# Performance work log

Hardware: AMD Instinct MI355X
Metric: run time of the kernel (lower is better)

## Reference

```python
import jax, jax.numpy as jnp
import numpy as np

B, C, H, W = 8, 256, 128, 128
J = 8          # number of segmentation classes / fc_mu layers
S = 256        # style_length
EPS = 1e-5


def _conv3x3(x, w, b):
    # x: [B,S,H,W], w: [C,S,3,3] (OIHW), padding=1 -> SAME
    y = jax.lax.conv_general_dilated(
        x, w, window_strides=(1, 1), padding='SAME',
        dimension_numbers=('NCHW', 'OIHW', 'NCHW'))
    return y + b[None, :, None, None]


def setup_inputs() -> dict:
    key = jax.random.key(0)
    ks = jax.random.split(key, 12)
    fp = jax.random.normal(ks[0], (B, C, H, W), dtype=jnp.float32)
    # one-hot segmentation map (nearest-interpolated seg maps are one-hot)
    labels = jax.random.randint(ks[1], (B, H, W), 0, J)
    sg = jnp.transpose(jax.nn.one_hot(labels, J, dtype=jnp.float32), (0, 3, 1, 2))
    style_codes = jax.random.normal(ks[2], (B, J + 1, S), dtype=jnp.float32)
    mask_codes = jax.random.randint(ks[3], (B, J), 0, 2).astype(jnp.int32)
    # parameters
    bn_weight = jnp.ones((C,), jnp.float32)
    bn_bias = jnp.zeros((C,), jnp.float32)
    conv_gamma_w = jax.random.normal(ks[4], (C, S, 3, 3), jnp.float32) * 0.02
    conv_gamma_b = jnp.zeros((C,), jnp.float32)
    conv_beta_w = jax.random.normal(ks[5], (C, S, 3, 3), jnp.float32) * 0.02
    conv_beta_b = jnp.zeros((C,), jnp.float32)
    fc_w = jax.random.normal(ks[6], (J, S, S), jnp.float32) * 0.02  # [j, out, in]
    fc_b = jnp.zeros((J, S), jnp.float32)
    return dict(fp=fp, sg=sg, style_codes=style_codes, mask_codes=mask_codes,
                bn_weight=bn_weight, bn_bias=bn_bias,
                conv_gamma_w=conv_gamma_w, conv_gamma_b=conv_gamma_b,
                conv_beta_w=conv_beta_w, conv_beta_b=conv_beta_b,
                fc_w=fc_w, fc_b=fc_b)


def reference(fp, sg, style_codes, mask_codes, bn_weight, bn_bias,
              conv_gamma_w, conv_gamma_b, conv_beta_w, conv_beta_b,
              fc_w, fc_b):
    # BatchNorm2d (training-mode batch statistics, affine)
    mean = jnp.mean(fp, axis=(0, 2, 3), keepdims=True)
    var = jnp.var(fp, axis=(0, 2, 3), keepdims=True)
    xn = (fp - mean) * jax.lax.rsqrt(var + EPS)
    xn = xn * bn_weight[None, :, None, None] + bn_bias[None, :, None, None]

    nJ = sg.shape[1]
    # style code selection: j if mask_codes[b,j]==1 else nJ (the extra/shared code)
    idx = jnp.where(mask_codes == 1, jnp.arange(nJ)[None, :], nJ)        # [B,J]
    codes = jnp.take_along_axis(style_codes, idx[:, :, None], axis=1)    # [B,J,S]
    # per-region Linear (weights differ per region j) + ReLU
    mu = jax.nn.relu(jnp.einsum('bjs,jts->bjt', codes, fc_w) + fc_b[None])  # [B,J,S]
    # masked scatter of per-region style vectors (sg is one-hot -> exact)
    middle = jnp.einsum('bjhw,bjs->bshw', sg, mu)                         # [B,S,H,W]

    gamma = _conv3x3(middle, conv_gamma_w, conv_gamma_b)
    beta = _conv3x3(middle, conv_beta_w, conv_beta_b)
    return xn * (1.0 + gamma) + beta
```

## Files before the change

kernel.cpp:

```cpp
#include <hip/hip_runtime.h>
#include <hip/hip_fp16.h>
#include <stdint.h>

#define NB 8
#define NC 256
#define NH 128
#define NW 128
#define NJ 8
#define NS 256
#define NHW (NH*NW)
#define BN_EPS 1e-5f
#define TSTRIDE 68

__device__ inline __half2 u2h(uint32_t u) {
    union { uint32_t u; __half2 h; } x; x.u = u; return x.h;
}
__device__ inline uint32_t h2u(__half2 h) {
    union { uint32_t u; __half2 h; } x; x.h = h; return x.u;
}

__global__ __launch_bounds__(256) void kA(
        const float* __restrict__ fp, float* __restrict__ psum, float* __restrict__ psq,
        const float* __restrict__ sg, uint8_t* __restrict__ lab,
        const float* __restrict__ style, const int* __restrict__ mask,
        const float* __restrict__ fcw, const float* __restrict__ fcb,
        float* __restrict__ mu,
        const float* __restrict__ wg, const float* __restrict__ wb,
        uint32_t* __restrict__ wpk) {
    __shared__ float ls[4], lq[4];
    __shared__ float code[NS];
    __shared__ uint32_t tileu[32][65];
    int blk = blockIdx.x;
    int t = threadIdx.x;
    if (blk < 512) {
        int pix = blk * 256 + t;
        int b = pix >> 14, hw = pix & 16383;
        const float* base = sg + (size_t)b * NJ * NHW + hw;
        int l = 0;
        #pragma unroll
        for (int j = 0; j < NJ; j++)
            if (base[(size_t)j * NHW] > 0.5f) l = j;
        lab[pix] = (uint8_t)l;
    } else if (blk < 576) {
        int bj = blk - 512;
        int b = bj >> 3, j = bj & 7;
        int row = (mask[bj] == 1) ? j : NJ;
        code[t] = style[((size_t)b * (NJ + 1) + row) * NS + t];
        __syncthreads();
        const float4* w4 = (const float4*)(fcw + ((size_t)j * NS + t) * NS);
        const float4* c4 = (const float4*)code;
        float acc = fcb[j * NS + t];
        for (int s4 = 0; s4 < NS / 4; s4++) {
            float4 wv = w4[s4];
            float4 cv = c4[s4];
            acc += wv.x * cv.x + wv.y * cv.y + wv.z * cv.z + wv.w * cv.w;
        }
        mu[bj * NS + t] = fmaxf(acc, 0.f);
    } else if (blk < 864) {
        int i = blk - 576;
        int skc = i % 72, cc = i / 72;
        int sk0 = skc * 32, c0 = cc * 64;
        {
            int skl = t & 31, cl = t >> 5;
            #pragma unroll
            for (int p = 0; p < 8; p++) {
                int c = c0 + cl + p * 8;
                float g  = __builtin_nontemporal_load(&wg[(size_t)c * 2304 + sk0 + skl]);
                float b2 = __builtin_nontemporal_load(&wb[(size_t)c * 2304 + sk0 + skl]);
                tileu[skl][cl + p * 8] = h2u(__floats2half2_rn(g, b2));
            }
        }
        __syncthreads();
        {
            int cl = t & 63, skl = t >> 6;
            #pragma unroll
            for (int p = 0; p < 8; p++) {
                int sk = sk0 + skl + p * 4;
                int s = sk / 9, k = sk - s * 9;
                wpk[(size_t)k * (NS * NC) + (size_t)s * NC + c0 + cl] = tileu[skl + p * 4][cl];
            }
        }
    } else {
        int bc = blk - 864;
        int b = bc >> 8, c = bc & 255;
        const float4* p = (const float4*)(fp + (size_t)(b * NC + c) * NHW);
        float s = 0.f, q = 0.f;
        for (int i = t; i < NHW / 4; i += 256) {
            float4 v = p[i];
            s += v.x + v.y + v.z + v.w;
            q += v.x * v.x + v.y * v.y + v.z * v.z + v.w * v.w;
        }
        for (int o = 32; o > 0; o >>= 1) {
            s += __shfl_down(s, o);
            q += __shfl_down(q, o);
        }
        int wid = t >> 6, lane = t & 63;
        if (lane == 0) { ls[wid] = s; lq[wid] = q; }
        __syncthreads();
        if (t == 0) {
            float S2 = 0.f, Q2 = 0.f;
            for (int i = 0; i < 4; i++) { S2 += ls[i]; Q2 += lq[i]; }
            psum[c * 8 + b] = S2;
            psq[c * 8 + b] = Q2;
        }
    }
}

__global__ __launch_bounds__(1024) void kB(
        const float* __restrict__ psum, const float* __restrict__ psq,
        const float* __restrict__ bnw, const float* __restrict__ bnb,
        const float* __restrict__ cgb, const float* __restrict__ cbb,
        float2* __restrict__ Al, uint32_t* __restrict__ Bl,
        const float* __restrict__ mu, const uint32_t* __restrict__ wpk,
        uint32_t* __restrict__ T) {
    int blk = blockIdx.x;
    int t = threadIdx.x;
    if (blk == 72) {
        if (t < 256) {
            int c = t;
            float s = 0.f, q = 0.f;
            for (int b = 0; b < NB; b++) { s += psum[c * 8 + b]; q += psq[c * 8 + b]; }
            const float N = (float)(NB * NHW);
            float mean = s / N;
            float var = q / N - mean * mean;
            if (var < 0.f) var = 0.f;
            float inv = 1.0f / sqrtf(var + BN_EPS);
            float a = bnw[c] * inv;
            float b2 = bnb[c] - mean * a;
            Al[c] = make_float2(a, b2);
            Bl[c] = h2u(__floats2half2_rn(1.0f + cgb[c], cbb[c]));
        }
        return;
    }
    int b = blk / 9, k = blk - b * 9;
    __shared__ float ms[NS * NJ];
    for (int i = t; i < NJ * NS; i += 1024) {
        int j = i >> 8, s = i & 255;
        ms[s * 8 + j] = mu[(size_t)b * NJ * NS + i];
    }
    __syncthreads();
    int c = t & 255, jq = t >> 8;
    int j0 = jq * 2;
    const uint32_t* wp = wpk + (size_t)k * NS * NC + c;
    float g0 = 0.f, be0 = 0.f, g1 = 0.f, be1 = 0.f;
    for (int s = 0; s < NS; s++) {
        float2 w2 = __half22float2(u2h(wp[(size_t)s * NC]));
        float2 mm = *(const float2*)&ms[s * 8 + j0];
        g0  += mm.x * w2.x;  be0 += mm.x * w2.y;
        g1  += mm.y * w2.x;  be1 += mm.y * w2.y;
    }
    uint32_t* o = T + ((size_t)b * 9 + k) * 9 * NC + c;
    o[(size_t)j0 * NC]       = h2u(__floats2half2_rn(g0, be0));
    o[(size_t)(j0 + 1) * NC] = h2u(__floats2half2_rn(g1, be1));
    if (jq == 0) o[(size_t)8 * NC] = 0u;
}

#define TAP_TREE(FLD, OUT)                                              \
    {                                                                   \
        __half2 p01 = __hadd2(u2h(tv[0].FLD), u2h(tv[1].FLD));          \
        __half2 p23 = __hadd2(u2h(tv[2].FLD), u2h(tv[3].FLD));          \
        __half2 p45 = __hadd2(u2h(tv[4].FLD), u2h(tv[5].FLD));          \
        __half2 p67 = __hadd2(u2h(tv[6].FLD), u2h(tv[7].FLD));          \
        __half2 p8b = __hadd2(u2h(tv[8].FLD), u2h(bias.FLD));           \
        OUT = __hadd2(__hadd2(__hadd2(p01, p23), __hadd2(p45, p67)), p8b); \
    }

__global__ __launch_bounds__(256, 5) void k_main(
        const float* __restrict__ fp, const uint8_t* __restrict__ lab,
        const uint32_t* __restrict__ T, const float2* __restrict__ Ag,
        const uint32_t* __restrict__ Bg, float* __restrict__ out) {
    int blk = blockIdx.x;
    int cc = blk & 3;
    int h  = (blk >> 2) & 127;
    int b  = blk >> 9;
    int c0 = cc * 64;

    __shared__ uint32_t Tl[81 * TSTRIDE];
    __shared__ float2   Apl[64];
    __shared__ uint32_t Bpl[64];
    __shared__ uint8_t  Ll[3][NW];

    int t = threadIdx.x;
    {
        const uint32_t* Tg = T + (size_t)b * 81 * NC + c0;
        int rr = t >> 4, ii = (t & 15) * 4;
        #pragma unroll
        for (int pass = 0; pass < 5; pass++) {
            int r = rr + pass * 16;
            *(uint4*)&Tl[r * TSTRIDE + ii] = *(const uint4*)&Tg[(size_t)r * NC + ii];
        }
        if (t < 16) *(uint4*)&Tl[80 * TSTRIDE + t * 4] = *(const uint4*)&Tg[(size_t)80 * NC + t * 4];
    }
    if (t < 64) { Apl[t] = Ag[c0 + t]; Bpl[t] = Bg[c0 + t]; }
    if (t >= 128 && t < 224) {
        int tt = t - 128;
        int r = tt >> 5, q = tt & 31;
        int hr = h - 1 + r;
        uint32_t v = 0;
        if (hr >= 0 && hr < NH)
            v = ((const uint32_t*)(lab + (size_t)b * NHW + (size_t)hr * NW))[q];
        ((uint32_t*)Ll)[tt] = v;
    }
    __syncthreads();

    int w = t & 127, cg = t >> 7;
    int base_k[9];
    #pragma unroll
    for (int dy = 0; dy < 3; dy++) {
        int hr = h - 1 + dy;
        bool rok = (hr >= 0) && (hr < NH);
        #pragma unroll
        for (int dx = 0; dx < 3; dx++) {
            int ww = w - 1 + dx;
            bool ok = rok && (ww >= 0) && (ww < NW);
            int wc = ww < 0 ? 0 : (ww > NW - 1 ? NW - 1 : ww);
            int j = ok ? (int)Ll[dy][wc] : 8;
            int k = dy * 3 + dx;
            base_k[k] = (k * 9 + j) * TSTRIDE + cg * 32;
        }
    }

    const float* fpb = fp + ((size_t)b * NC + c0 + cg * 32) * NHW + (size_t)h * NW + w;
    float*       ob  = out + ((size_t)b * NC + c0 + cg * 32) * NHW + (size_t)h * NW + w;

    #pragma unroll
    for (int q = 0; q < 8; q++) {
        float x0 = fpb[(size_t)(q * 4 + 0) * NHW];
        float x1 = fpb[(size_t)(q * 4 + 1) * NHW];
        float x2 = fpb[(size_t)(q * 4 + 2) * NHW];
        float x3 = fpb[(size_t)(q * 4 + 3) * NHW];
        uint4 tv[9];
        #pragma unroll
        for (int k = 0; k < 9; k++)
            tv[k] = *(const uint4*)&Tl[base_k[k] + q * 4];
        uint4 bias = *(const uint4*)&Bpl[cg * 32 + q * 4];
        __half2 a0, a1, a2, a3;
        TAP_TREE(x, a0);
        TAP_TREE(y, a1);
        TAP_TREE(z, a2);
        TAP_TREE(w, a3);
        float4 ap01 = *(const float4*)&Apl[cg * 32 + q * 4];
        float4 ap23 = *(const float4*)&Apl[cg * 32 + q * 4 + 2];
        float2 g0 = __half22float2(a0);
        float2 g1 = __half22float2(a1);
        float2 g2 = __half22float2(a2);
        float2 g3 = __half22float2(a3);
        __builtin_nontemporal_store((x0 * ap01.x + ap01.y) * g0.x + g0.y, &ob[(size_t)(q * 4 + 0) * NHW]);
        __builtin_nontemporal_store((x1 * ap01.z + ap01.w) * g1.x + g1.y, &ob[(size_t)(q * 4 + 1) * NHW]);
        __builtin_nontemporal_store((x2 * ap23.x + ap23.y) * g2.x + g2.y, &ob[(size_t)(q * 4 + 2) * NHW]);
        __builtin_nontemporal_store((x3 * ap23.z + ap23.w) * g3.x + g3.y, &ob[(size_t)(q * 4 + 3) * NHW]);
    }
}

extern "C" void kernel_launch(void* const* d_in, const int* in_sizes, int n_in,
                              void* d_out, int out_size, void* d_ws, size_t ws_size,
                              hipStream_t stream) {
    const float* fp    = (const float*)d_in[0];
    const float* sg    = (const float*)d_in[1];
    const float* style = (const float*)d_in[2];
    const int*   mask  = (const int*)d_in[3];
    const float* bnw   = (const float*)d_in[4];
    const float* bnb   = (const float*)d_in[5];
    const float* cgw   = (const float*)d_in[6];
    const float* cgb   = (const float*)d_in[7];
    const float* cbw   = (const float*)d_in[8];
    const float* cbb   = (const float*)d_in[9];
    const float* fcw   = (const float*)d_in[10];
    const float* fcb   = (const float*)d_in[11];
    float* out = (float*)d_out;

    char* ws = (char*)d_ws;
    float*    psum = (float*)(ws + 0);
    float*    psq  = (float*)(ws + 8192);
    float2*   Al   = (float2*)(ws + 16384);
    uint32_t* Bl   = (uint32_t*)(ws + 18432);
    uint8_t*  lab  = (uint8_t*)(ws + 19456);
    float*    mu   = (float*)(ws + 150528);
    uint32_t* wpk  = (uint32_t*)(ws + 216064);
    uint32_t* T    = (uint32_t*)(ws + 2575360);

    hipLaunchKernelGGL(kA, dim3(2912), dim3(256), 0, stream,
                       fp, psum, psq, sg, lab, style, mask, fcw, fcb, mu,
                       cgw, cbw, wpk);
    hipLaunchKernelGGL(kB, dim3(73), dim3(1024), 0, stream,
                       psum, psq, bnw, bnb, cgb, cbb, Al, Bl, mu, wpk, T);
    hipLaunchKernelGGL(k_main, dim3(NB * NH * 4), dim3(256), 0, stream,
                       fp, lab, T, Al, Bl, out);
}
```

Before: 85.13 us.

## Split conv-tap table between LDS and global loads, add nontemporal hints

Moves the last three of the nine conv-tap table rows out of shared memory, loading them per thread straight from global/L2 with a one-step software prefetch across the q loop. This shrinks the LDS staging footprint and the LDS read traffic per output, aiming for more occupancy and less LDS-bound time. The cost is extra global gathers and more registers. Separately, the label and FC-weight reads in the prologue kernel now use nontemporal loads.

```diff
diff --git a/kernel.cpp b/kernel.cpp
--- a/kernel.cpp
+++ b/kernel.cpp
@@ -11,6 +11,8 @@
 #define NHW (NH*NW)
 #define BN_EPS 1e-5f
 #define TSTRIDE 68
+
+typedef float f4v __attribute__((ext_vector_type(4)));
 
 __device__ inline __half2 u2h(uint32_t u) {
     union { uint32_t u; __half2 h; } x; x.u = u; return x.h;
@@ -39,7 +41,7 @@
         int l = 0;
         #pragma unroll
         for (int j = 0; j < NJ; j++)
-            if (base[(size_t)j * NHW] > 0.5f) l = j;
+            if (__builtin_nontemporal_load(&base[(size_t)j * NHW]) > 0.5f) l = j;
         lab[pix] = (uint8_t)l;
     } else if (blk < 576) {
         int bj = blk - 512;
@@ -47,12 +49,12 @@
         int row = (mask[bj] == 1) ? j : NJ;
         code[t] = style[((size_t)b * (NJ + 1) + row) * NS + t];
         __syncthreads();
-        const float4* w4 = (const float4*)(fcw + ((size_t)j * NS + t) * NS);
-        const float4* c4 = (const float4*)code;
+        const f4v* w4 = (const f4v*)(fcw + ((size_t)j * NS + t) * NS);
+        const f4v* c4 = (const f4v*)code;
         float acc = fcb[j * NS + t];
         for (int s4 = 0; s4 < NS / 4; s4++) {
-            float4 wv = w4[s4];
-            float4 cv = c4[s4];
+            f4v wv = __builtin_nontemporal_load(&w4[s4]);
+            f4v cv = c4[s4];
             acc += wv.x * cv.x + wv.y * cv.y + wv.z * cv.z + wv.w * cv.w;
         }
         mu[bj * NS + t] = fmaxf(acc, 0.f);
@@ -160,8 +162,8 @@
         __half2 p01 = __hadd2(u2h(tv[0].FLD), u2h(tv[1].FLD));          \
         __half2 p23 = __hadd2(u2h(tv[2].FLD), u2h(tv[3].FLD));          \
         __half2 p45 = __hadd2(u2h(tv[4].FLD), u2h(tv[5].FLD));          \
-        __half2 p67 = __hadd2(u2h(tv[6].FLD), u2h(tv[7].FLD));          \
-        __half2 p8b = __hadd2(u2h(tv[8].FLD), u2h(bias.FLD));           \
+        __half2 p67 = __hadd2(u2h(gt0.FLD), u2h(gt1.FLD));              \
+        __half2 p8b = __hadd2(u2h(gt2.FLD), u2h(bias.FLD));             \
         OUT = __hadd2(__hadd2(__hadd2(p01, p23), __hadd2(p45, p67)), p8b); \
     }
 
@@ -175,21 +177,18 @@
     int b  = blk >> 9;
     int c0 = cc * 64;
 
-    __shared__ uint32_t Tl[81 * TSTRIDE];
+    __shared__ uint32_t Tl[54 * TSTRIDE];
     __shared__ float2   Apl[64];
     __shared__ uint32_t Bpl[64];
     __shared__ uint8_t  Ll[3][NW];
 
     int t = threadIdx.x;
+    const uint32_t* Tg = T + (size_t)b * 81 * NC;
     {
-        const uint32_t* Tg = T + (size_t)b * 81 * NC + c0;
+        const uint32_t* Ts = Tg + c0;
         int rr = t >> 4, ii = (t & 15) * 4;
-        #pragma unroll
-        for (int pass = 0; pass < 5; pass++) {
-            int r = rr + pass * 16;
-            *(uint4*)&Tl[r * TSTRIDE + ii] = *(const uint4*)&Tg[(size_t)r * NC + ii];
-        }
-        if (t < 16) *(uint4*)&Tl[80 * TSTRIDE + t * 4] = *(const uint4*)&Tg[(size_t)80 * NC + t * 4];
+        for (int r = rr; r < 54; r += 16)
+            *(uint4*)&Tl[r * TSTRIDE + ii] = *(const uint4*)&Ts[(size_t)r * NC + ii];
     }
     if (t < 64) { Apl[t] = Ag[c0 + t]; Bpl[t] = Bg[c0 + t]; }
     if (t >= 128 && t < 224) {
@@ -204,7 +203,8 @@
     __syncthreads();
 
     int w = t & 127, cg = t >> 7;
-    int base_k[9];
+    int base_k[6];
+    uint32_t goff[3];
     #pragma unroll
     for (int dy = 0; dy < 3; dy++) {
         int hr = h - 1 + dy;
@@ -216,22 +216,34 @@
             int wc = ww < 0 ? 0 : (ww > NW - 1 ? NW - 1 : ww);
             int j = ok ? (int)Ll[dy][wc] : 8;
             int k = dy * 3 + dx;
-            base_k[k] = (k * 9 + j) * TSTRIDE + cg * 32;
-        }
-    }
-
+            if (k < 6) base_k[k] = (k * 9 + j) * TSTRIDE + cg * 32;
+            else goff[k - 6] = (uint32_t)(((k * 9 + j) * NC + c0 + cg * 32) * 4);
+        }
+    }
+
+    const char* Tgb = (const char*)Tg;
     const float* fpb = fp + ((size_t)b * NC + c0 + cg * 32) * NHW + (size_t)h * NW + w;
     float*       ob  = out + ((size_t)b * NC + c0 + cg * 32) * NHW + (size_t)h * NW + w;
 
+    uint4 gt0 = *(const uint4*)(Tgb + goff[0]);
+    uint4 gt1 = *(const uint4*)(Tgb + goff[1]);
+    uint4 gt2 = *(const uint4*)(Tgb + goff[2]);
+
     #pragma unroll
     for (int q = 0; q < 8; q++) {
+        uint4 n0 = gt0, n1 = gt1, n2 = gt2;
+        if (q < 7) {
+            n0 = *(const uint4*)(Tgb + goff[0] + (q + 1) * 16);
+            n1 = *(const uint4*)(Tgb + goff[1] + (q + 1) * 16);
+            n2 = *(const uint4*)(Tgb + goff[2] + (q + 1) * 16);
+        }
         float x0 = fpb[(size_t)(q * 4 + 0) * NHW];
         float x1 = fpb[(size_t)(q * 4 + 1) * NHW];
         float x2 = fpb[(size_t)(q * 4 + 2) * NHW];
         float x3 = fpb[(size_t)(q * 4 + 3) * NHW];
-        uint4 tv[9];
+        uint4 tv[6];
         #pragma unroll
-        for (int k = 0; k < 9; k++)
+        for (int k = 0; k < 6; k++)
             tv[k] = *(const uint4*)&Tl[base_k[k] + q * 4];
         uint4 bias = *(const uint4*)&Bpl[cg * 32 + q * 4];
         __half2 a0, a1, a2, a3;
@@ -249,6 +261,7 @@
         __builtin_nontemporal_store((x1 * ap01.z + ap01.w) * g1.x + g1.y, &ob[(size_t)(q * 4 + 1) * NHW]);
         __builtin_nontemporal_store((x2 * ap23.x + ap23.y) * g2.x + g2.y, &ob[(size_t)(q * 4 + 2) * NHW]);
         __builtin_nontemporal_store((x3 * ap23.z + ap23.w) * g3.x + g3.y, &ob[(size_t)(q * 4 + 3) * NHW]);
+        gt0 = n0; gt1 = n1; gt2 = n2;
     }
 }
 
```

New measurement: 109.4 us. 1.29x slower.
